# Kernel optimization log

Measured on AMD Instinct MI355X. Metric: run time of the kernel, lower is better.

The kernel has to match this reference:

```python
import jax, jax.numpy as jnp
import numpy as np

# ---- constants from init_kwargs ----
RES = 128                       # config.grid.resolution (base_resolution, n_levels=1)
LOG2_T = 22
TABLE_SIZE = 1 << LOG2_T        # hashmap entries
N_G = 4                         # features per level, gaussian grid
N_V = 8                         # features per level, vmf grid
BB_MIN = jnp.array([-10.0, -10.0, -10.0], dtype=jnp.float32)
BB_MAX = jnp.array([10.0, 10.0, 10.0], dtype=jnp.float32)
N_PTS = 1048576

_P2 = np.uint32(2654435761)
_P3 = np.uint32(805459861)
# 8 trilinear corner offsets [8,3]
_CORNERS = jnp.array([[i, j, k] for i in (0, 1) for j in (0, 1) for k in (0, 1)], dtype=jnp.int32)


def hashgrid_lookup(table, pos):
    """tcnn-style HashGrid (1 level, trilinear). pos: [N,3] in [0,1] domain."""
    x = pos * RES                     # scale to grid coords
    x0 = jnp.floor(x)
    w = x - x0                        # [N,3] trilinear weights
    corners = x0.astype(jnp.int32)[:, None, :] + _CORNERS[None]   # [N,8,3]
    cu = corners.astype(jnp.uint32)
    h = (cu[..., 0] ^ (cu[..., 1] * _P2) ^ (cu[..., 2] * _P3)) & jnp.uint32(TABLE_SIZE - 1)
    feat = table[h.astype(jnp.int32)]                              # [N,8,F] gather
    wts = jnp.prod(jnp.where(_CORNERS[None].astype(bool), w[:, None, :], 1.0 - w[:, None, :]), axis=-1)  # [N,8]
    return jnp.einsum('nc,ncf->nf', wts, feat)                     # [N,F]


def sample_vpls(pos, gauss_table, vmf_table):
    """Accumulate encodings over the 27-neighbor stencil (accumulate_gaussians=True)."""
    block = 1.0 / RES
    npos = (pos - BB_MIN) / (BB_MAX - BB_MIN)      # normalized [N,3]
    total_g = jnp.zeros((pos.shape[0], N_G), dtype=jnp.float32)
    total_v = jnp.zeros((pos.shape[0], N_V), dtype=jnp.float32)
    for dx in (-1, 0, 1):
        for dy in (-1, 0, 1):
            for dz in (-1, 0, 1):
                off = jnp.array([dx, dy, dz], dtype=jnp.float32) * block
                p = npos + off
                total_g = total_g + hashgrid_lookup(gauss_table, p)
                total_v = total_v + hashgrid_lookup(vmf_table, p)
    return total_g, total_v


def encode(gaussians, vmf):
    # gaussian_mean_encoding='sigmoid' (non-raw -> rescale to bbox)
    mean = jax.nn.sigmoid(gaussians[:, :3]) * (BB_MAX - BB_MIN) + BB_MIN
    variance = jax.nn.softplus(gaussians[:, 3])[:, None]          # 'softplus'
    sharpness = jnp.exp(vmf[:, 0])[:, None]                        # 'exp'
    ax = vmf[:, 1:4]                                               # 'normalize' (F.normalize, eps=1e-12)
    axis = ax / jnp.maximum(jnp.linalg.norm(ax, axis=1, keepdims=True), 1e-12)
    amplitude = jax.nn.sigmoid(vmf[:, 4:7])                        # 'sigmoid'
    g_out = jnp.concatenate([mean, variance], axis=1)             # [N,4]
    v_out = jnp.concatenate([sharpness, axis, amplitude], axis=1) # [N,7]
    return g_out, v_out


def setup_inputs() -> dict:
    key = jax.random.key(0)
    k1, k2, k3 = jax.random.split(key, 3)
    # world-space query positions inside the bounding box
    u = jax.random.uniform(k1, (N_PTS, 3), dtype=jnp.float32)
    pos = u * (BB_MAX - BB_MIN) + BB_MIN
    # hash-grid feature tables (tcnn initializes near zero)
    gauss_table = jax.random.normal(k2, (TABLE_SIZE, N_G), dtype=jnp.float32) * 0.1
    vmf_table = jax.random.normal(k3, (TABLE_SIZE, N_V), dtype=jnp.float32) * 0.1
    return {"pos": pos, "gauss_table": gauss_table, "vmf_table": vmf_table}


def reference(pos, gauss_table, vmf_table):
    gaussians, vmf = sample_vpls(pos, gauss_table, vmf_table)
    return encode(gaussians, vmf)
```

## Files before the change

### kernel.cpp

```cpp
#include <hip/hip_runtime.h>
#include <hip/hip_fp16.h>
#include <cstdint>

#define TABLE_MASK 0x3FFFFFu
#define P2 2654435761u
#define P3 805459861u

#define XD 128
#define YD 132
#define ZD 132
#define RECU 12
#define NB3 (128 * 128 * 8)
#define SCAN_BLKS (NB3 / 1024)
#define BUILD_BLKS (131 * 66)

__device__ __forceinline__ float sigmoidf_(float x) { return 1.0f / (1.0f + expf(-x)); }

__device__ __forceinline__ uint32_t f2h2(float a, float b) {
    __half2 h = __floats2half2_rn(a, b);
    return *reinterpret_cast<uint32_t*>(&h);
}
__device__ __forceinline__ __half2 u2h2(uint32_t u) {
    return *reinterpret_cast<__half2*>(&u);
}

__device__ __forceinline__ int bin_key3(float px, float py, float pz)
{
    float x = ((px + 10.0f) / 20.0f) * 128.0f;
    float y = ((py + 10.0f) / 20.0f) * 128.0f;
    float z = ((pz + 10.0f) / 20.0f) * 128.0f;
    int ix = min(max((int)floorf(x), 0), 127);
    int iy = min(max((int)floorf(y), 0), 127);
    int iz = min(max((int)floorf(z), 0), 127);
    return (((iz << 7) + iy) << 3) + (ix >> 4);
}

__global__ __launch_bounds__(256)
void build_hist_kernel(const float4* __restrict__ gauss,
                       const float4* __restrict__ vmf,
                       uint32_t* __restrict__ exdx,
                       const float* __restrict__ pos,
                       uint32_t* __restrict__ hist, int n)
{
    if (blockIdx.x >= BUILD_BLKS) {
        int p = (blockIdx.x - BUILD_BLKS) * blockDim.x + threadIdx.x;
        if (p < n) {
            int k = bin_key3(pos[3 * p], pos[3 * p + 1], pos[3 * p + 2]);
            atomicAdd(&hist[k], 1u);
        }
        return;
    }

    __shared__ float sm[2][131][13];
    int bidx = blockIdx.x;
    int yp = bidx % 66;
    int rz = 1 + bidx / 66;
    int ry0 = 1 + 2 * yp;
    int t = threadIdx.x;

    for (int l = t; l < 262; l += 256) {
        int row = (l >= 131) ? 1 : 0;
        int cell = l - row * 131;
        int ry = ry0 + row;
        if (ry <= 131) {
            int xc = 1 + cell;
            uint32_t ux = (uint32_t)(xc - 2);
            uint32_t uy = (uint32_t)(ry - 2);
            uint32_t uz = (uint32_t)(rz - 2);
            uint32_t h = (ux ^ (uy * P2) ^ (uz * P3)) & TABLE_MASK;
            float4 g  = gauss[h];
            float4 v0 = vmf[(size_t)2 * h];
            float4 v1 = vmf[(size_t)2 * h + 1];
            float* s = sm[row][cell];
            s[0] = g.x;  s[1] = g.y;  s[2]  = g.z;  s[3]  = g.w;
            s[4] = v0.x; s[5] = v0.y; s[6]  = v0.z; s[7]  = v0.w;
            s[8] = v1.x; s[9] = v1.y; s[10] = v1.z; s[11] = v1.w;
        }
    }
    __syncthreads();

    int row = t >> 7;
    int c   = t & 127;
    int ry  = ry0 + row;
    if (ry > 131) return;

    uint32_t rec[12];
#pragma unroll
    for (int m = 0; m < 6; ++m) {
        float e0 = sm[row][c][2*m]   + sm[row][c+1][2*m]   + sm[row][c+2][2*m];
        float e1 = sm[row][c][2*m+1] + sm[row][c+1][2*m+1] + sm[row][c+2][2*m+1];
        float d0 = sm[row][c+3][2*m]   - sm[row][c][2*m];
        float d1 = sm[row][c+3][2*m+1] - sm[row][c][2*m+1];
        rec[m]     = f2h2(e0, e1);
        rec[6 + m] = f2h2(d0, d1);
    }
    size_t o = (((size_t)rz * YD + (size_t)ry) * XD + (size_t)c) * RECU;
    *(uint4*)(exdx + o)     = make_uint4(rec[0], rec[1], rec[2],  rec[3]);
    *(uint4*)(exdx + o + 4) = make_uint4(rec[4], rec[5], rec[6],  rec[7]);
    *(uint4*)(exdx + o + 8) = make_uint4(rec[8], rec[9], rec[10], rec[11]);
}

__global__ __launch_bounds__(1024)
void scanA_kernel(const uint32_t* __restrict__ hist,
                  uint32_t* __restrict__ cursor,
                  uint32_t* __restrict__ sums)
{
    __shared__ uint32_t buf[1024];
    int t = threadIdx.x;
    int base = blockIdx.x * 1024;
    uint32_t v = hist[base + t];
    buf[t] = v;
    __syncthreads();
    for (int off = 1; off < 1024; off <<= 1) {
        uint32_t x = (t >= off) ? buf[t - off] : 0u;
        __syncthreads();
        buf[t] += x;
        __syncthreads();
    }
    cursor[base + t] = buf[t] - v;
    if (t == 1023) sums[blockIdx.x] = buf[t];
}

__global__ __launch_bounds__(256)
void scatter_kernel(const float* __restrict__ pos,
                    uint32_t* __restrict__ cursor,
                    const uint32_t* __restrict__ sums,
                    float4* __restrict__ sortedPts, int n)
{
    __shared__ uint32_t soff[SCAN_BLKS];
    int t = threadIdx.x;
    if (t < SCAN_BLKS) soff[t] = sums[t];
    __syncthreads();
    for (int off = 1; off < SCAN_BLKS; off <<= 1) {
        uint32_t v = 0;
        if (t < SCAN_BLKS && t >= off) v = soff[t - off];
        __syncthreads();
        if (t < SCAN_BLKS) soff[t] += v;
        __syncthreads();
    }

    int p = blockIdx.x * blockDim.x + t;
    if (p >= n) return;
    float px = pos[3 * p], py = pos[3 * p + 1], pz = pos[3 * p + 2];
    int k = bin_key3(px, py, pz);
    int chunk = k >> 10;
    uint32_t base = (chunk > 0) ? soff[chunk - 1] : 0u;
    uint32_t slot = base + atomicAdd(&cursor[k], 1u);
    sortedPts[slot] = make_float4(px, py, pz, __uint_as_float((uint32_t)p));
}

__device__ __forceinline__ void consume_cell(const uint4& v0, const uint4& v1, const uint4& v2,
                                             __half2 wxh, float w, float* acc)
{
    __half2 t; float2 f;
    t = __hfma2(wxh, u2h2(v1.z), u2h2(v0.x)); f = __half22float2(t);
    acc[0] = fmaf(w, f.x, acc[0]); acc[1] = fmaf(w, f.y, acc[1]);
    t = __hfma2(wxh, u2h2(v1.w), u2h2(v0.y)); f = __half22float2(t);
    acc[2] = fmaf(w, f.x, acc[2]); acc[3] = fmaf(w, f.y, acc[3]);
    t = __hfma2(wxh, u2h2(v2.x), u2h2(v0.z)); f = __half22float2(t);
    acc[4] = fmaf(w, f.x, acc[4]); acc[5] = fmaf(w, f.y, acc[5]);
    t = __hfma2(wxh, u2h2(v2.y), u2h2(v0.w)); f = __half22float2(t);
    acc[6] = fmaf(w, f.x, acc[6]); acc[7] = fmaf(w, f.y, acc[7]);
    t = __hfma2(wxh, u2h2(v2.z), u2h2(v1.x)); f = __half22float2(t);
    acc[8] = fmaf(w, f.x, acc[8]); acc[9] = fmaf(w, f.y, acc[9]);
    t = __hfma2(wxh, u2h2(v2.w), u2h2(v1.y)); f = __half22float2(t);
    acc[10] = fmaf(w, f.x, acc[10]); acc[11] = fmaf(w, f.y, acc[11]);
}

__global__ __launch_bounds__(256, 8)
void vapl_grid_sorted_kernel(const float4* __restrict__ sortedPts,
                             const uint32_t* __restrict__ exdx,
                             float* __restrict__ out,
                             int n)
{
    int bid = blockIdx.x;
    int nb  = gridDim.x;
    int b2  = ((nb & 7) == 0) ? ((bid & 7) * (nb >> 3) + (bid >> 3)) : bid;
    int s = b2 * (int)blockDim.x + (int)threadIdx.x;
    if (s >= n) return;

    float4 pt = sortedPts[s];
    int p = (int)__float_as_uint(pt.w);

    float x = ((pt.x + 10.0f) / 20.0f) * 128.0f;
    float y = ((pt.y + 10.0f) / 20.0f) * 128.0f;
    float z = ((pt.z + 10.0f) / 20.0f) * 128.0f;

    float fx = floorf(x), fy = floorf(y), fz = floorf(z);
    int ix = (int)fx, iy = (int)fy, iz = (int)fz;
    float wx = x - fx, wy = y - fy, wz = z - fz;

    float ay[4] = {1.0f - wy, 1.0f, 1.0f, wy};
    float az[4] = {1.0f - wz, 1.0f, 1.0f, wz};
    __half2 wxh = __float2half2_rn(wx);

    int bx = ix + 1, by = iy + 1, bz = iz + 1;

    float acc[12] = {0.f,0.f,0.f,0.f,0.f,0.f,0.f,0.f,0.f,0.f,0.f,0.f};

#pragma unroll
    for (int k = 0; k < 4; ++k) {
        float azk = az[k];
        const uint32_t* rowb = exdx +
            (((size_t)(bz + k) * YD + (size_t)by) * XD + (size_t)(bx - 1)) * RECU;
#pragma unroll
        for (int j = 0; j < 4; ++j) {
            const uint32_t* r = rowb + (size_t)j * (XD * RECU);
            float w = ay[j] * azk;
            uint4 v0 = *(const uint4*)(r);
            uint4 v1 = *(const uint4*)(r + 4);
            uint4 v2 = *(const uint4*)(r + 8);
            consume_cell(v0, v1, v2, wxh, w, acc);
        }
    }

    float m0 = sigmoidf_(acc[0]) * 20.0f - 10.0f;
    float m1 = sigmoidf_(acc[1]) * 20.0f - 10.0f;
    float m2 = sigmoidf_(acc[2]) * 20.0f - 10.0f;
    float var = fmaxf(acc[3], 0.0f) + log1pf(expf(-fabsf(acc[3])));

    float sharp = expf(acc[4]);
    float nrm = fmaxf(sqrtf(acc[5]*acc[5] + acc[6]*acc[6] + acc[7]*acc[7]), 1e-12f);
    float a0 = acc[5] / nrm, a1 = acc[6] / nrm, a2 = acc[7] / nrm;
    float amp0 = sigmoidf_(acc[8]);
    float amp1 = sigmoidf_(acc[9]);
    float amp2 = sigmoidf_(acc[10]);

    *(float4*)(out + (size_t)p * 4) = make_float4(m0, m1, m2, var);

    float* ov = out + (size_t)n * 4 + (size_t)p * 7;
    ov[0] = sharp;
    ov[1] = a0;
    ov[2] = a1;
    ov[3] = a2;
    ov[4] = amp0;
    ov[5] = amp1;
    ov[6] = amp2;
}

__global__ __launch_bounds__(256)
void vapl_grid_kernel(const float* __restrict__ pos,
                      const float4* __restrict__ gauss,
                      const float4* __restrict__ vmf,
                      float* __restrict__ out,
                      int n)
{
    int p = blockIdx.x * blockDim.x + threadIdx.x;
    if (p >= n) return;

    float px = pos[3 * p + 0];
    float py = pos[3 * p + 1];
    float pz = pos[3 * p + 2];

    float x = ((px + 10.0f) / 20.0f) * 128.0f;
    float y = ((py + 10.0f) / 20.0f) * 128.0f;
    float z = ((pz + 10.0f) / 20.0f) * 128.0f;

    float fx = floorf(x), fy = floorf(y), fz = floorf(z);
    int ix = (int)fx, iy = (int)fy, iz = (int)fz;
    float wx = x - fx, wy = y - fy, wz = z - fz;

    float ax[4] = {1.0f - wx, 1.0f, 1.0f, wx};
    float ay[4] = {1.0f - wy, 1.0f, 1.0f, wy};
    float az[4] = {1.0f - wz, 1.0f, 1.0f, wz};

    uint32_t hx[4], hy[4], hz[4];
#pragma unroll
    for (int i = 0; i < 4; ++i) {
        hx[i] = (uint32_t)(ix - 1 + i);
        hy[i] = (uint32_t)(iy - 1 + i) * P2;
        hz[i] = (uint32_t)(iz - 1 + i) * P3;
    }

    float tg0 = 0.f, tg1 = 0.f, tg2 = 0.f, tg3 = 0.f;
    float tv0 = 0.f, tv1 = 0.f, tv2 = 0.f, tv3 = 0.f;
    float tv4 = 0.f, tv5 = 0.f, tv6 = 0.f, tv7 = 0.f;

    for (int k = 0; k < 4; ++k) {
        for (int j = 0; j < 4; ++j) {
            uint32_t hyz = hy[j] ^ hz[k];
            float wyz = ay[j] * az[k];
#pragma unroll
            for (int i = 0; i < 4; ++i) {
                uint32_t h = (hx[i] ^ hyz) & TABLE_MASK;
                float w = ax[i] * wyz;
                float4 g  = gauss[h];
                float4 v0 = vmf[(size_t)2 * h];
                float4 v1 = vmf[(size_t)2 * h + 1];
                tg0 = fmaf(w, g.x,  tg0);
                tg1 = fmaf(w, g.y,  tg1);
                tg2 = fmaf(w, g.z,  tg2);
                tg3 = fmaf(w, g.w,  tg3);
                tv0 = fmaf(w, v0.x, tv0);
                tv1 = fmaf(w, v0.y, tv1);
                tv2 = fmaf(w, v0.z, tv2);
                tv3 = fmaf(w, v0.w, tv3);
                tv4 = fmaf(w, v1.x, tv4);
                tv5 = fmaf(w, v1.y, tv5);
                tv6 = fmaf(w, v1.z, tv6);
                tv7 = fmaf(w, v1.w, tv7);
            }
        }
    }

    float m0 = sigmoidf_(tg0) * 20.0f - 10.0f;
    float m1 = sigmoidf_(tg1) * 20.0f - 10.0f;
    float m2 = sigmoidf_(tg2) * 20.0f - 10.0f;
    float var = fmaxf(tg3, 0.0f) + log1pf(expf(-fabsf(tg3)));

    float sharp = expf(tv0);
    float nrm = fmaxf(sqrtf(tv1 * tv1 + tv2 * tv2 + tv3 * tv3), 1e-12f);
    float a0 = tv1 / nrm, a1 = tv2 / nrm, a2 = tv3 / nrm;
    float amp0 = sigmoidf_(tv4);
    float amp1 = sigmoidf_(tv5);
    float amp2 = sigmoidf_(tv6);

    float* og = out + (size_t)p * 4;
    og[0] = m0;
    og[1] = m1;
    og[2] = m2;
    og[3] = var;

    float* ov = out + (size_t)n * 4 + (size_t)p * 7;
    ov[0] = sharp;
    ov[1] = a0;
    ov[2] = a1;
    ov[3] = a2;
    ov[4] = amp0;
    ov[5] = amp1;
    ov[6] = amp2;
}

extern "C" void kernel_launch(void* const* d_in, const int* in_sizes, int n_in,
                              void* d_out, int out_size, void* d_ws, size_t ws_size,
                              hipStream_t stream) {
    const float*  pos   = (const float*)d_in[0];
    const float4* gauss = (const float4*)d_in[1];
    const float4* vmf   = (const float4*)d_in[2];
    float* out = (float*)d_out;
    int n = in_sizes[0] / 3;

    size_t off = 0;
    char* ws = (char*)d_ws;
    uint32_t* exdx   = (uint32_t*)(ws + off);  off += (size_t)XD * YD * ZD * RECU * 4;
    off = (off + 255) & ~(size_t)255;
    uint32_t* hist   = (uint32_t*)(ws + off);  off += (size_t)NB3 * 4;
    uint32_t* cursor = (uint32_t*)(ws + off);  off += (size_t)NB3 * 4;
    uint32_t* sums   = (uint32_t*)(ws + off);  off += 256 * 4;
    off = (off + 255) & ~(size_t)255;
    float4* sortedPts = (float4*)(ws + off);   off += (size_t)n * 16;
    const size_t need = off;

    dim3 block(256);
    dim3 grid((n + 255) / 256);

    if (ws_size >= need) {
        (void)hipMemsetAsync(hist, 0, (size_t)NB3 * 4, stream);
        hipLaunchKernelGGL(build_hist_kernel, dim3(BUILD_BLKS + 4096), block, 0, stream,
                           gauss, vmf, exdx, pos, hist, n);
        hipLaunchKernelGGL(scanA_kernel, dim3(SCAN_BLKS), dim3(1024), 0, stream, hist, cursor, sums);
        hipLaunchKernelGGL(scatter_kernel, grid, block, 0, stream, pos, cursor, sums, sortedPts, n);
        hipLaunchKernelGGL(vapl_grid_sorted_kernel, grid, block, 0, stream,
                           sortedPts, exdx, out, n);
    } else {
        hipLaunchKernelGGL(vapl_grid_kernel, grid, block, 0, stream, pos, gauss, vmf, out, n);
    }
}
```

Baseline: 259.2 us.

## Sort build rows by hash region and fuse table build with scatter

Adds a block to the histogram kernel that counting-sorts the 17161 (y,z) grid rows by the high bits of their base hash, so the table-build blocks process rows whose gathers land in nearby table regions. The gather-heavy table build then moves into the same launch as the point scatter, so the two overlap on the device. This aims for better cache locality on hash-table reads and fewer serialized phases. In exchange it adds a single-block row sort and an extra workspace buffer, and the build now runs after the scan instead of beside the histogram.

```diff
diff --git a/kernel.cpp b/kernel.cpp
--- a/kernel.cpp
+++ b/kernel.cpp
@@ -12,7 +12,8 @@
 #define RECU 12
 #define NB3 (128 * 128 * 8)
 #define SCAN_BLKS (NB3 / 1024)
-#define BUILD_BLKS (131 * 66)
+#define NROWS 17161
+#define NBUILD ((NROWS + 1) / 2)
 
 __device__ __forceinline__ float sigmoidf_(float x) { return 1.0f / (1.0f + expf(-x)); }
 
@@ -36,14 +37,13 @@
 }
 
 __global__ __launch_bounds__(256)
-void build_hist_kernel(const float4* __restrict__ gauss,
-                       const float4* __restrict__ vmf,
-                       uint32_t* __restrict__ exdx,
-                       const float* __restrict__ pos,
-                       uint32_t* __restrict__ hist, int n)
-{
-    if (blockIdx.x >= BUILD_BLKS) {
-        int p = (blockIdx.x - BUILD_BLKS) * blockDim.x + threadIdx.x;
+void hist_rowsort_kernel(const float* __restrict__ pos,
+                         uint32_t* __restrict__ hist,
+                         uint32_t* __restrict__ rowOrder, int n)
+{
+    int t = threadIdx.x;
+    if (blockIdx.x < 4096) {
+        int p = blockIdx.x * 256 + t;
         if (p < n) {
             int k = bin_key3(pos[3 * p], pos[3 * p + 1], pos[3 * p + 2]);
             atomicAdd(&hist[k], 1u);
@@ -51,38 +51,126 @@
         return;
     }
 
+    __shared__ uint32_t histL[1024];
+    __shared__ uint32_t part[256];
+    for (int i = t; i < 1024; i += 256) histL[i] = 0u;
+    __syncthreads();
+    for (int l = t; l < NROWS; l += 256) {
+        int ry = 1 + (l % 131), rz = 1 + (l / 131);
+        uint32_t key = (((uint32_t)(ry - 2)) * P2 ^ ((uint32_t)(rz - 2)) * P3) & TABLE_MASK;
+        atomicAdd(&histL[key >> 12], 1u);
+    }
+    __syncthreads();
+    uint32_t s0 = histL[4*t], s1 = histL[4*t+1], s2 = histL[4*t+2], s3 = histL[4*t+3];
+    uint32_t tot = s0 + s1 + s2 + s3;
+    part[t] = tot;
+    __syncthreads();
+    for (int off = 1; off < 256; off <<= 1) {
+        uint32_t v = (t >= off) ? part[t - off] : 0u;
+        __syncthreads();
+        part[t] += v;
+        __syncthreads();
+    }
+    uint32_t base = part[t] - tot;
+    histL[4*t]   = base;
+    histL[4*t+1] = base + s0;
+    histL[4*t+2] = base + s0 + s1;
+    histL[4*t+3] = base + s0 + s1 + s2;
+    __syncthreads();
+    for (int l = t; l < NROWS; l += 256) {
+        int ry = 1 + (l % 131), rz = 1 + (l / 131);
+        uint32_t key = (((uint32_t)(ry - 2)) * P2 ^ ((uint32_t)(rz - 2)) * P3) & TABLE_MASK;
+        uint32_t slot = atomicAdd(&histL[key >> 12], 1u);
+        rowOrder[slot] = ((uint32_t)rz << 8) | (uint32_t)ry;
+    }
+}
+
+__global__ __launch_bounds__(1024)
+void scanA_kernel(const uint32_t* __restrict__ hist,
+                  uint32_t* __restrict__ cursor,
+                  uint32_t* __restrict__ sums)
+{
+    __shared__ uint32_t buf[1024];
+    int t = threadIdx.x;
+    int base = blockIdx.x * 1024;
+    uint32_t v = hist[base + t];
+    buf[t] = v;
+    __syncthreads();
+    for (int off = 1; off < 1024; off <<= 1) {
+        uint32_t x = (t >= off) ? buf[t - off] : 0u;
+        __syncthreads();
+        buf[t] += x;
+        __syncthreads();
+    }
+    cursor[base + t] = buf[t] - v;
+    if (t == 1023) sums[blockIdx.x] = buf[t];
+}
+
+__global__ __launch_bounds__(256)
+void build_scatter_kernel(const float4* __restrict__ gauss,
+                          const float4* __restrict__ vmf,
+                          uint32_t* __restrict__ exdx,
+                          const uint32_t* __restrict__ rowOrder,
+                          const float* __restrict__ pos,
+                          uint32_t* __restrict__ cursor,
+                          const uint32_t* __restrict__ sums,
+                          float4* __restrict__ sortedPts, int n)
+{
     __shared__ float sm[2][131][13];
-    int bidx = blockIdx.x;
-    int yp = bidx % 66;
-    int rz = 1 + bidx / 66;
-    int ry0 = 1 + 2 * yp;
+    __shared__ uint32_t soff[SCAN_BLKS];
     int t = threadIdx.x;
+
+    if (blockIdx.x >= NBUILD) {
+        if (t < SCAN_BLKS) soff[t] = sums[t];
+        __syncthreads();
+        for (int off = 1; off < SCAN_BLKS; off <<= 1) {
+            uint32_t v = 0;
+            if (t < SCAN_BLKS && t >= off) v = soff[t - off];
+            __syncthreads();
+            if (t < SCAN_BLKS) soff[t] += v;
+            __syncthreads();
+        }
+        int p = (blockIdx.x - NBUILD) * 256 + t;
+        if (p >= n) return;
+        float px = pos[3 * p], py = pos[3 * p + 1], pz = pos[3 * p + 2];
+        int k = bin_key3(px, py, pz);
+        int chunk = k >> 10;
+        uint32_t base = (chunk > 0) ? soff[chunk - 1] : 0u;
+        uint32_t slot = base + atomicAdd(&cursor[k], 1u);
+        sortedPts[slot] = make_float4(px, py, pz, __uint_as_float((uint32_t)p));
+        return;
+    }
+
+    int b = blockIdx.x;
+    uint32_t r0v = rowOrder[2 * b];
+    bool has1 = (2 * b + 1 < NROWS);
+    uint32_t r1v = has1 ? rowOrder[2 * b + 1] : r0v;
 
     for (int l = t; l < 262; l += 256) {
         int row = (l >= 131) ? 1 : 0;
+        if (row && !has1) continue;
         int cell = l - row * 131;
-        int ry = ry0 + row;
-        if (ry <= 131) {
-            int xc = 1 + cell;
-            uint32_t ux = (uint32_t)(xc - 2);
-            uint32_t uy = (uint32_t)(ry - 2);
-            uint32_t uz = (uint32_t)(rz - 2);
-            uint32_t h = (ux ^ (uy * P2) ^ (uz * P3)) & TABLE_MASK;
-            float4 g  = gauss[h];
-            float4 v0 = vmf[(size_t)2 * h];
-            float4 v1 = vmf[(size_t)2 * h + 1];
-            float* s = sm[row][cell];
-            s[0] = g.x;  s[1] = g.y;  s[2]  = g.z;  s[3]  = g.w;
-            s[4] = v0.x; s[5] = v0.y; s[6]  = v0.z; s[7]  = v0.w;
-            s[8] = v1.x; s[9] = v1.y; s[10] = v1.z; s[11] = v1.w;
-        }
+        uint32_t rv = row ? r1v : r0v;
+        int ry = (int)(rv & 0xFF), rz = (int)(rv >> 8);
+        uint32_t ux = (uint32_t)(cell - 1);
+        uint32_t uy = (uint32_t)(ry - 2);
+        uint32_t uz = (uint32_t)(rz - 2);
+        uint32_t h = (ux ^ (uy * P2) ^ (uz * P3)) & TABLE_MASK;
+        float4 g  = gauss[h];
+        float4 v0 = vmf[(size_t)2 * h];
+        float4 v1 = vmf[(size_t)2 * h + 1];
+        float* s = sm[row][cell];
+        s[0] = g.x;  s[1] = g.y;  s[2]  = g.z;  s[3]  = g.w;
+        s[4] = v0.x; s[5] = v0.y; s[6]  = v0.z; s[7]  = v0.w;
+        s[8] = v1.x; s[9] = v1.y; s[10] = v1.z; s[11] = v1.w;
     }
     __syncthreads();
 
     int row = t >> 7;
     int c   = t & 127;
-    int ry  = ry0 + row;
-    if (ry > 131) return;
+    if (row && !has1) return;
+    uint32_t rv = row ? r1v : r0v;
+    int ry = (int)(rv & 0xFF), rz = (int)(rv >> 8);
 
     uint32_t rec[12];
 #pragma unroll
@@ -98,55 +186,6 @@
     *(uint4*)(exdx + o)     = make_uint4(rec[0], rec[1], rec[2],  rec[3]);
     *(uint4*)(exdx + o + 4) = make_uint4(rec[4], rec[5], rec[6],  rec[7]);
     *(uint4*)(exdx + o + 8) = make_uint4(rec[8], rec[9], rec[10], rec[11]);
-}
-
-__global__ __launch_bounds__(1024)
-void scanA_kernel(const uint32_t* __restrict__ hist,
-                  uint32_t* __restrict__ cursor,
-                  uint32_t* __restrict__ sums)
-{
-    __shared__ uint32_t buf[1024];
-    int t = threadIdx.x;
-    int base = blockIdx.x * 1024;
-    uint32_t v = hist[base + t];
-    buf[t] = v;
-    __syncthreads();
-    for (int off = 1; off < 1024; off <<= 1) {
-        uint32_t x = (t >= off) ? buf[t - off] : 0u;
-        __syncthreads();
-        buf[t] += x;
-        __syncthreads();
-    }
-    cursor[base + t] = buf[t] - v;
-    if (t == 1023) sums[blockIdx.x] = buf[t];
-}
-
-__global__ __launch_bounds__(256)
-void scatter_kernel(const float* __restrict__ pos,
-                    uint32_t* __restrict__ cursor,
-                    const uint32_t* __restrict__ sums,
-                    float4* __restrict__ sortedPts, int n)
-{
-    __shared__ uint32_t soff[SCAN_BLKS];
-    int t = threadIdx.x;
-    if (t < SCAN_BLKS) soff[t] = sums[t];
-    __syncthreads();
-    for (int off = 1; off < SCAN_BLKS; off <<= 1) {
-        uint32_t v = 0;
-        if (t < SCAN_BLKS && t >= off) v = soff[t - off];
-        __syncthreads();
-        if (t < SCAN_BLKS) soff[t] += v;
-        __syncthreads();
-    }
-
-    int p = blockIdx.x * blockDim.x + t;
-    if (p >= n) return;
-    float px = pos[3 * p], py = pos[3 * p + 1], pz = pos[3 * p + 2];
-    int k = bin_key3(px, py, pz);
-    int chunk = k >> 10;
-    uint32_t base = (chunk > 0) ? soff[chunk - 1] : 0u;
-    uint32_t slot = base + atomicAdd(&cursor[k], 1u);
-    sortedPts[slot] = make_float4(px, py, pz, __uint_as_float((uint32_t)p));
 }
 
 __device__ __forceinline__ void consume_cell(const uint4& v0, const uint4& v1, const uint4& v2,
@@ -342,13 +381,14 @@
 
     size_t off = 0;
     char* ws = (char*)d_ws;
-    uint32_t* exdx   = (uint32_t*)(ws + off);  off += (size_t)XD * YD * ZD * RECU * 4;
+    uint32_t* exdx     = (uint32_t*)(ws + off);  off += (size_t)XD * YD * ZD * RECU * 4;
     off = (off + 255) & ~(size_t)255;
-    uint32_t* hist   = (uint32_t*)(ws + off);  off += (size_t)NB3 * 4;
-    uint32_t* cursor = (uint32_t*)(ws + off);  off += (size_t)NB3 * 4;
-    uint32_t* sums   = (uint32_t*)(ws + off);  off += 256 * 4;
+    uint32_t* hist     = (uint32_t*)(ws + off);  off += (size_t)NB3 * 4;
+    uint32_t* cursor   = (uint32_t*)(ws + off);  off += (size_t)NB3 * 4;
+    uint32_t* sums     = (uint32_t*)(ws + off);  off += 256 * 4;
+    uint32_t* rowOrder = (uint32_t*)(ws + off);  off += (size_t)NROWS * 4;
     off = (off + 255) & ~(size_t)255;
-    float4* sortedPts = (float4*)(ws + off);   off += (size_t)n * 16;
+    float4* sortedPts  = (float4*)(ws + off);    off += (size_t)n * 16;
     const size_t need = off;
 
     dim3 block(256);
@@ -356,10 +396,11 @@
 
     if (ws_size >= need) {
         (void)hipMemsetAsync(hist, 0, (size_t)NB3 * 4, stream);
-        hipLaunchKernelGGL(build_hist_kernel, dim3(BUILD_BLKS + 4096), block, 0, stream,
-                           gauss, vmf, exdx, pos, hist, n);
+        hipLaunchKernelGGL(hist_rowsort_kernel, dim3(4097), block, 0, stream,
+                           pos, hist, rowOrder, n);
         hipLaunchKernelGGL(scanA_kernel, dim3(SCAN_BLKS), dim3(1024), 0, stream, hist, cursor, sums);
-        hipLaunchKernelGGL(scatter_kernel, grid, block, 0, stream, pos, cursor, sums, sortedPts, n);
+        hipLaunchKernelGGL(build_scatter_kernel, dim3(NBUILD + 4096), block, 0, stream,
+                           gauss, vmf, exdx, rowOrder, pos, cursor, sums, sortedPts, n);
         hipLaunchKernelGGL(vapl_grid_sorted_kernel, grid, block, 0, stream,
                            sortedPts, exdx, out, n);
     } else {
```

Measured after the change: 263.4 us. No clear change (+1.6%).
